# Kernel optimization log

Hardware: AMD Instinct MI355X
Metric: run time of the kernel (lower is better)

The kernel has to match this reference:

```python
import jax, jax.numpy as jnp
import numpy as np

N_NODES = 20000
N_EDGES = 160000
N_GRAPHS = 1000
IN_DIM = 11
HID = 128
EDGE_DIM = 3
N_LAYERS = 5
BN_EPS = 1e-5


def setup_inputs() -> dict:
    key = jax.random.key(0)
    ks = jax.random.split(key, 24)
    x = jax.random.normal(ks[0], (N_NODES, IN_DIM), dtype=jnp.float32)
    edge_index = jax.random.randint(ks[1], (2, N_EDGES), 0, N_NODES, dtype=jnp.int64)
    batch = jnp.sort(jax.random.randint(ks[2], (N_NODES,), 0, N_GRAPHS, dtype=jnp.int64))
    edge_attr = jax.random.uniform(ks[3], (N_EDGES, EDGE_DIM), dtype=jnp.float32)
    s_in = 1.0 / np.sqrt(IN_DIM)
    s_z = 1.0 / np.sqrt(2 * HID + EDGE_DIM)
    s_h = 1.0 / np.sqrt(HID)
    W_in = jax.random.uniform(ks[4], (IN_DIM, HID), minval=-s_in, maxval=s_in)
    b_in = jax.random.uniform(ks[5], (HID,), minval=-s_in, maxval=s_in)
    Wf = jax.random.uniform(ks[6], (N_LAYERS, 2 * HID + EDGE_DIM, HID), minval=-s_z, maxval=s_z)
    bf = jax.random.uniform(ks[7], (N_LAYERS, HID), minval=-s_z, maxval=s_z)
    Ws = jax.random.uniform(ks[8], (N_LAYERS, 2 * HID + EDGE_DIM, HID), minval=-s_z, maxval=s_z)
    bs = jax.random.uniform(ks[9], (N_LAYERS, HID), minval=-s_z, maxval=s_z)
    gamma = jnp.ones((N_LAYERS, HID), dtype=jnp.float32)
    beta = jnp.zeros((N_LAYERS, HID), dtype=jnp.float32)
    W1 = jax.random.uniform(ks[10], (HID, HID), minval=-s_h, maxval=s_h)
    b1 = jax.random.uniform(ks[11], (HID,), minval=-s_h, maxval=s_h)
    W2 = jax.random.uniform(ks[12], (HID, HID), minval=-s_h, maxval=s_h)
    b2 = jax.random.uniform(ks[13], (HID,), minval=-s_h, maxval=s_h)
    W3 = jax.random.uniform(ks[14], (HID, 1), minval=-s_h, maxval=s_h)
    b3 = jax.random.uniform(ks[15], (1,), minval=-s_h, maxval=s_h)
    return {"x": x, "edge_index": edge_index, "batch": batch, "edge_attr": edge_attr,
            "W_in": W_in, "b_in": b_in, "Wf": Wf, "bf": bf, "Ws": Ws, "bs": bs,
            "gamma": gamma, "beta": beta, "W1": W1, "b1": b1, "W2": W2, "b2": b2,
            "W3": W3, "b3": b3}


def reference(x, edge_index, batch, edge_attr, W_in, b_in, Wf, bf, Ws, bs,
              gamma, beta, W1, b1, W2, b2, W3, b3):
    src = edge_index[0]  # x_j (source / neighbor)
    dst = edge_index[1]  # x_i (target / aggregation index)
    # in-degree per node for mean aggregation (zero-degree -> divide by 1, yields 0)
    deg = jax.ops.segment_sum(jnp.ones((N_EDGES,), jnp.float32), dst, num_segments=N_NODES)
    deg = jnp.maximum(deg, 1.0)[:, None]

    h = x @ W_in + b_in  # [N, H]
    for l in range(N_LAYERS):
        # CGConv: z = [x_i, x_j, e]; msg = sigmoid(z Wf) * softplus(z Ws); residual + mean-aggr
        z = jnp.concatenate([h[dst], h[src], edge_attr], axis=-1)  # [E, 2H+D]
        msg = jax.nn.sigmoid(z @ Wf[l] + bf[l]) * jax.nn.softplus(z @ Ws[l] + bs[l])
        agg = jax.ops.segment_sum(msg, dst, num_segments=N_NODES) / deg
        h = h + agg
        # BatchNorm1d (training-mode batch stats, biased variance)
        mu = jnp.mean(h, axis=0)
        var = jnp.mean((h - mu) ** 2, axis=0)
        h = (h - mu) * jax.lax.rsqrt(var + BN_EPS) * gamma[l] + beta[l]
        h = jax.nn.relu(h)
        # dropout omitted (eval mode)

    # global mean pool over graphs
    cnt = jax.ops.segment_sum(jnp.ones((N_NODES,), jnp.float32), batch, num_segments=N_GRAPHS)
    g = jax.ops.segment_sum(h, batch, num_segments=N_GRAPHS) / jnp.maximum(cnt, 1.0)[:, None]

    g = jax.nn.relu(g @ W1 + b1)
    g = jax.nn.relu(g @ W2 + b2)
    return g @ W3 + b3  # [G, 1]
```

## Files before the change

### kernel.cpp

```cpp
#include <hip/hip_runtime.h>
#include <hip/hip_cooperative_groups.h>
#include <math.h>

namespace cg = cooperative_groups;

#define NN 20000
#define NE 160000
#define NG 1000
#define IND 11
#define H 128
#define ED 3
#define NL 5
#define ZDH (259*128)
#define BN_EPSF 1e-5f
#define EPW 32
#define QR 16
#define GP 4
#define MBLK 313
#define NWIN (NE / EPW)
#define MEGA_BLOCKS 1024

#define DEG_BLKS ((NE + 255) / 256)
#define WPREP_BLKS ((NL * 512 * H + 255) / 256)
#define GB_BLKS ((NN + 255) / 256)
#define HIN_BLKS 512
#define PREP_ITEMS (DEG_BLKS + WPREP_BLKS + GB_BLKS + HIN_BLKS)
#define RSV_ITEMS ((NN + 255) / 256)
#define SCAT_ITEMS ((NE + 255) / 256)
#define ZERO_INTS (NN + 1 + NE / 32)

typedef unsigned short ushort_t;
typedef unsigned int uint_t;
typedef __attribute__((ext_vector_type(8))) short bf8_t;
typedef __attribute__((ext_vector_type(4))) float f4_t;

__device__ inline ushort_t f2bf(float x) {
    unsigned int u = __float_as_uint(x);
    unsigned int r = (u + 0x7fffu + ((u >> 16) & 1u)) >> 16;
    return (ushort_t)r;
}
__device__ inline float bf2f(ushort_t b) {
    return __uint_as_float(((unsigned int)b) << 16);
}


__device__ __forceinline__ void prep_item(int b, int tid,
                                          const int* __restrict__ dst,
                                          int* __restrict__ degi,
                                          const float* __restrict__ Wf,
                                          const float* __restrict__ Ws,
                                          ushort_t* __restrict__ Wt,
                                          const float* __restrict__ x,
                                          const float* __restrict__ Win,
                                          const float* __restrict__ bin,
                                          float* __restrict__ h,
                                          const int* __restrict__ batch,
                                          int* __restrict__ gstart,
                                          float* lw ) {
    if (b < DEG_BLKS) {
        int e = b * 256 + tid;
        if (e < NE) atomicAdd(&degi[dst[e]], 1);
    } else if (b < DEG_BLKS + WPREP_BLKS) {
        int idx = (b - DEG_BLKS) * 256 + tid;
        if (idx < NL * 512 * H) {
            int k = idx & 127;
            int n = (idx >> 7) & 511;
            int l = idx >> 16;
            int t = n >> 7, j = n & 127;
            const float* W = (t == 0 || t == 2) ? Wf : Ws;
            int krow = (t < 2) ? k : (H + k);
            ushort_t val = f2bf(W[(size_t)l * ZDH + krow * H + j]);
            int nt = j >> 4, sub = j & 15;
            int ks = k >> 5, quad = (k >> 3) & 3, e2 = k & 7;
            int lane = quad * 16 + sub;
            Wt[(size_t)l * 65536 + (size_t)t * 16384 +
               (((nt * 4 + ks) * 64 + lane) * 8 + e2)] = val;
        }
    } else if (b < DEG_BLKS + WPREP_BLKS + GB_BLKS) {
        int n = (b - DEG_BLKS - WPREP_BLKS) * 256 + tid;
        if (n < NN) {
            int b0 = batch[n];
            int bn = (n + 1 < NN) ? batch[n + 1] : NG;
            if (n == 0)
                for (int t = 0; t <= b0; ++t) gstart[t] = 0;
            for (int t = b0 + 1; t <= bn; ++t) gstart[t] = n + 1;
        }
    } else {
        for (int i = tid; i < IND * H; i += 256) lw[i] = Win[i];
        __syncthreads();
        int j = tid & 127;
        float bj = bin[j];
        int rb = b - (DEG_BLKS + WPREP_BLKS + GB_BLKS);
        for (int n = rb * 2 + (tid >> 7); n < NN; n += HIN_BLKS * 2) {
            const float* xr = x + (size_t)n * IND;
            float acc = bj;
#pragma unroll
            for (int k = 0; k < IND; ++k) acc = fmaf(xr[k], lw[k * H + j], acc);
            h[(size_t)n * H + j] = acc;
        }
    }
}

__device__ __forceinline__ void reserve_item(int b, int tid,
                                             const int* __restrict__ degi,
                                             int* __restrict__ cursor,
                                             float* __restrict__ invdeg,
                                             int* __restrict__ counter,
                                             unsigned* __restrict__ endmask) {
    int n = b * 256 + tid;
    int lane = tid & 63;
    int v = (n < NN) ? degi[n] : 0;
    int x = v;
#pragma unroll
    for (int st = 1; st < 64; st <<= 1) {
        int y = __shfl_up(x, st, 64);
        if (lane >= st) x += y;
    }
    int total = __shfl(x, 63, 64);
    int base = 0;
    if (lane == 63) base = atomicAdd(counter, total);
    base = __shfl(base, 63, 64);
    if (n < NN) {
        int st0 = base + x - v;
        cursor[n] = st0;
        invdeg[n] = 1.0f / (float)(v < 1 ? 1 : v);
        if (v > 0) {
            int endp = st0 + v - 1;
            atomicOr(&endmask[endp >> 5], 1u << (endp & 31));
        }
    }
}

__device__ __forceinline__ void scatter_item(int b, int tid,
                                             const int* __restrict__ src,
                                             const int* __restrict__ dst,
                                             const float* __restrict__ ea,
                                             const float* __restrict__ invdeg,
                                             int* __restrict__ cursor,
                                             float4* __restrict__ csr_ea4,
                                             int* __restrict__ csr_dst,
                                             float* __restrict__ csr_inv) {
    int e = b * 256 + tid;
    if (e < NE) {
        int d = dst[e];
        int pos = atomicAdd(&cursor[d], 1);
        float4 r;
        r.x = ea[e * ED + 0];
        r.y = ea[e * ED + 1];
        r.z = ea[e * ED + 2];
        r.w = __int_as_float(src[e]);
        csr_ea4[pos] = r;
        csr_dst[pos] = d;
        csr_inv[pos] = invdeg[d];
    }
}

__device__ __forceinline__ void gemm_item(int mb, int pair,
                                          const float* __restrict__ hsrc,
                                          float* __restrict__ hbn,
                                          const ushort_t* __restrict__ Wt_l,
                                          const float* bnsc, const float* bnsh,
                                          int applyBN,
                                          uint_t* __restrict__ ppack,
                                          uint_t* __restrict__ qpack, int tid) {
    int wave = tid >> 6;
    int lane = tid & 63;
    int sub = lane & 15;
    int quad = lane >> 4;
    int m0 = mb * 64 + wave * 16;
    int writeH = applyBN && (pair == 0);

    const bf8_t* fragF = (const bf8_t*)(Wt_l + (size_t)(2 * pair) * 16384);
    const bf8_t* fragS = (const bf8_t*)(Wt_l + (size_t)(2 * pair + 1) * 16384);

    bf8_t aHi[4], aLo[4];
    int r = m0 + sub;
    int rc = r < NN ? r : NN - 1;
#pragma unroll
    for (int ks = 0; ks < 4; ++ks) {
        int kb = ks * 32 + quad * 8;
        const float* hp = hsrc + (size_t)rc * H + kb;
        float4 v0 = *(const float4*)hp;
        float4 v1 = *(const float4*)(hp + 4);
        float vv[8] = {v0.x, v0.y, v0.z, v0.w, v1.x, v1.y, v1.z, v1.w};
        if (applyBN) {
#pragma unroll
            for (int i = 0; i < 8; ++i) {
                float v = fmaf(vv[i], bnsc[kb + i], bnsh[kb + i]);
                vv[i] = v > 0.0f ? v : 0.0f;
            }
        }
        bf8_t hi8, lo8;
#pragma unroll
        for (int i = 0; i < 8; ++i) {
            ushort_t hi = f2bf(vv[i]);
            hi8[i] = (short)hi;
            lo8[i] = (short)f2bf(vv[i] - bf2f(hi));
        }
        aHi[ks] = hi8;
        aLo[ks] = lo8;
        if (writeH && r < NN) {
            float* op = hbn + (size_t)r * H + kb;
            *(float4*)op = make_float4(vv[0], vv[1], vv[2], vv[3]);
            *(float4*)(op + 4) = make_float4(vv[4], vv[5], vv[6], vv[7]);
        }
    }

    f4_t accF[8], accS[8];
#pragma unroll
    for (int b = 0; b < 8; ++b) { accF[b] = (f4_t){0.f, 0.f, 0.f, 0.f}; accS[b] = (f4_t){0.f, 0.f, 0.f, 0.f}; }

#pragma unroll
    for (int nt = 0; nt < 8; ++nt) {
#pragma unroll
        for (int ks = 0; ks < 4; ++ks) {
            bf8_t bF = fragF[(nt * 4 + ks) * 64 + lane];
            bf8_t bS = fragS[(nt * 4 + ks) * 64 + lane];
            accF[nt] = __builtin_amdgcn_mfma_f32_16x16x32_bf16(aHi[ks], bF, accF[nt], 0, 0, 0);
            accF[nt] = __builtin_amdgcn_mfma_f32_16x16x32_bf16(aLo[ks], bF, accF[nt], 0, 0, 0);
            accS[nt] = __builtin_amdgcn_mfma_f32_16x16x32_bf16(aHi[ks], bS, accS[nt], 0, 0, 0);
            accS[nt] = __builtin_amdgcn_mfma_f32_16x16x32_bf16(aLo[ks], bS, accS[nt], 0, 0, 0);
        }
    }

    uint_t* outp = pair ? qpack : ppack;
#pragma unroll
    for (int nt = 0; nt < 8; ++nt) {
        int col = nt * 16 + sub;
#pragma unroll
        for (int rr = 0; rr < 4; ++rr) {
            int row = m0 + quad * 4 + rr;
            if (row < NN) {
                uint_t lo = f2bf(accF[nt][rr]);
                uint_t hi = f2bf(accS[nt][rr]);
                outp[(size_t)row * H + col] = lo | (hi << 16);
            }
        }
    }
}

struct AggW { float2 wf0, wf1, wf2, ws0, ws1, ws2, bfv, bsv; };

__device__ __forceinline__ AggW load_aggw(const float* __restrict__ Wf_l,
                                          const float* __restrict__ bf_l,
                                          const float* __restrict__ Ws_l,
                                          const float* __restrict__ bs_l, int c0) {
    AggW a;
    a.wf0 = *(const float2*)&Wf_l[256 * H + c0];
    a.wf1 = *(const float2*)&Wf_l[257 * H + c0];
    a.wf2 = *(const float2*)&Wf_l[258 * H + c0];
    a.ws0 = *(const float2*)&Ws_l[256 * H + c0];
    a.ws1 = *(const float2*)&Ws_l[257 * H + c0];
    a.ws2 = *(const float2*)&Ws_l[258 * H + c0];
    a.bfv = *(const float2*)&bf_l[c0];
    a.bsv = *(const float2*)&bs_l[c0];
    return a;
}

__device__ __forceinline__ void agg_window(int base,
                                           const int4* __restrict__ csr_fe,
                                           const int* __restrict__ csr_dst,
                                           const float* __restrict__ csr_inv,
                                           const unsigned* __restrict__ endmask,
                                           const AggW& aw,
                                           const uint_t* __restrict__ ppack,
                                           const uint_t* __restrict__ qpack,
                                           float* __restrict__ h, int lane) {
    int c0 = 2 * lane;
    int4 fe = csr_fe[base + (lane & (EPW - 1))];
    int  dd = csr_dst[base + (lane & (EPW - 1))];
    int  ivr = __float_as_int(csr_inv[base + (lane & (EPW - 1))]);
    unsigned mask = __builtin_amdgcn_readfirstlane(endmask[base >> 5]);

    uint2 q[QR];
#pragma unroll
    for (int i = 0; i < QR; ++i) {
        int s = __builtin_amdgcn_readlane(fe.w, i);
        q[i] = *(const uint2*)&qpack[(size_t)s * H + c0];
    }

    int dcur = __builtin_amdgcn_readlane(dd, 0);
    uint2 ppc = *(const uint2*)&ppack[(size_t)dcur * H + c0];
    float pf0 = __uint_as_float(ppc.x << 16) + aw.bfv.x;
    float ps0 = __uint_as_float(ppc.x & 0xFFFF0000u) + aw.bsv.x;
    float pf1 = __uint_as_float(ppc.y << 16) + aw.bfv.y;
    float ps1 = __uint_as_float(ppc.y & 0xFFFF0000u) + aw.bsv.y;
    unsigned m = mask;
    int e0 = m ? __builtin_ctz(m) : EPW;
    int dnext = 0;
    uint2 ppN = ppc;
    if (e0 + 1 < EPW) {
        dnext = __builtin_amdgcn_readlane(dd, e0 + 1);
        ppN = *(const uint2*)&ppack[(size_t)dnext * H + c0];
    }

    float acc0 = 0.f, acc1 = 0.f;

#pragma unroll
    for (int tb = 0; tb < EPW; tb += 8) {
#pragma unroll
        for (int i = 0; i < 8; ++i) {
            int t = tb + i;
            float ex = __int_as_float(__builtin_amdgcn_readlane(fe.x, t));
            float ey = __int_as_float(__builtin_amdgcn_readlane(fe.y, t));
            float ez = __int_as_float(__builtin_amdgcn_readlane(fe.z, t));
            uint2 qq = q[t & (QR - 1)];
            if (t + QR < EPW) {
                int s2 = __builtin_amdgcn_readlane(fe.w, t + QR);
                q[t & (QR - 1)] = *(const uint2*)&qpack[(size_t)s2 * H + c0];
            }
            float qf0 = __uint_as_float(qq.x << 16);
            float qs0 = __uint_as_float(qq.x & 0xFFFF0000u);
            float qf1 = __uint_as_float(qq.y << 16);
            float qs1 = __uint_as_float(qq.y & 0xFFFF0000u);
            float f0 = fmaf(ex, aw.wf0.x, fmaf(ey, aw.wf1.x, fmaf(ez, aw.wf2.x, pf0 + qf0)));
            float v0 = fmaf(ex, aw.ws0.x, fmaf(ey, aw.ws1.x, fmaf(ez, aw.ws2.x, ps0 + qs0)));
            float f1 = fmaf(ex, aw.wf0.y, fmaf(ey, aw.wf1.y, fmaf(ez, aw.wf2.y, pf1 + qf1)));
            float v1 = fmaf(ex, aw.ws0.y, fmaf(ey, aw.ws1.y, fmaf(ez, aw.ws2.y, ps1 + qs1)));
            float sig0 = __builtin_amdgcn_rcpf(1.0f + __expf(-f0));
            float sp0  = fmaxf(v0, 0.0f) + __logf(1.0f + __expf(-fabsf(v0)));
            float sig1 = __builtin_amdgcn_rcpf(1.0f + __expf(-f1));
            float sp1  = fmaxf(v1, 0.0f) + __logf(1.0f + __expf(-fabsf(v1)));
            acc0 = fmaf(sig0, sp0, acc0);
            acc1 = fmaf(sig1, sp1, acc1);
            if (mask & (1u << t)) {
                float inv = __int_as_float(__builtin_amdgcn_readlane(ivr, t));
                atomicAdd(&h[(size_t)dcur * H + c0], acc0 * inv);
                atomicAdd(&h[(size_t)dcur * H + c0 + 1], acc1 * inv);
                acc0 = 0.f; acc1 = 0.f;
                dcur = dnext;
                pf0 = __uint_as_float(ppN.x << 16) + aw.bfv.x;
                ps0 = __uint_as_float(ppN.x & 0xFFFF0000u) + aw.bsv.x;
                pf1 = __uint_as_float(ppN.y << 16) + aw.bfv.y;
                ps1 = __uint_as_float(ppN.y & 0xFFFF0000u) + aw.bsv.y;
                m &= m - 1;
                int e1 = m ? __builtin_ctz(m) : EPW;
                if (e1 + 1 < EPW) {
                    dnext = __builtin_amdgcn_readlane(dd, e1 + 1);
                    ppN = *(const uint2*)&ppack[(size_t)dnext * H + c0];
                }
            }
        }
    }
    if (!(mask & (1u << (EPW - 1)))) {
        float inv = __int_as_float(__builtin_amdgcn_readlane(ivr, EPW - 1));
        atomicAdd(&h[(size_t)dcur * H + c0], acc0 * inv);
        atomicAdd(&h[(size_t)dcur * H + c0 + 1], acc1 * inv);
    }
}

__device__ __forceinline__ void stats_part(const float* __restrict__ h,
                                           float* __restrict__ sum,
                                           float* __restrict__ sumsq,
                                           int j, int part, int nparts) {
    float s = 0.0f, ss = 0.0f;
    for (int n = part * 8; n + 7 < NN; n += nparts * 8) {
        float v[8];
#pragma unroll
        for (int i = 0; i < 8; ++i) v[i] = h[(size_t)(n + i) * H + j];
#pragma unroll
        for (int i = 0; i < 8; ++i) { s += v[i]; ss = fmaf(v[i], v[i], ss); }
    }
    atomicAdd(&sum[j], s);
    atomicAdd(&sumsq[j], ss);
}

__global__ __launch_bounds__(256, 4) void mega_kernel(
        const int* __restrict__ src, const int* __restrict__ dst,
        const float* __restrict__ ea, const float* __restrict__ x,
        const float* __restrict__ Win, const float* __restrict__ bin,
        const int* __restrict__ batch,
        int* __restrict__ degi, int* __restrict__ counter,
        unsigned* __restrict__ endmask, int* __restrict__ cursor,
        float* __restrict__ invdeg, float4* __restrict__ csr_ea4,
        int* __restrict__ csr_dst, float* __restrict__ csr_inv,
        int* __restrict__ gstart,
        const float* __restrict__ Wf, const float* __restrict__ bf,
        const float* __restrict__ Ws, const float* __restrict__ bs,
        ushort_t* __restrict__ Wt,
        float* __restrict__ hA, float* __restrict__ hB,
        uint_t* __restrict__ ppack, uint_t* __restrict__ qpack,
        float* __restrict__ sum, float* __restrict__ sumsq,
        const float* __restrict__ gamma, const float* __restrict__ beta,
        const float* __restrict__ W1, const float* __restrict__ b1,
        const float* __restrict__ W2, const float* __restrict__ b2,
        const float* __restrict__ W3, const float* __restrict__ b3,
        float* __restrict__ out) {
    cg::grid_group grid = cg::this_grid();
    __shared__ float bnsc[H];
    __shared__ float bnsh[H];
    __shared__ float lw[IND * H];
    __shared__ float s1[GP][H];
    __shared__ float s2[GP][H];
    __shared__ float wred[2][GP];
    int tid = threadIdx.x;
    int lane = tid & 63;
    int wv = tid >> 6;

    for (int i = blockIdx.x * 256 + tid; i < ZERO_INTS; i += gridDim.x * 256)
        degi[i] = 0;
    grid.sync();

    for (int item = blockIdx.x; item < PREP_ITEMS; item += gridDim.x) {
        prep_item(item, tid, dst, degi, Wf, Ws, Wt, x, Win, bin, hA, batch,
                  gstart, lw);
        __syncthreads();
    }
    grid.sync();

    for (int item = blockIdx.x; item < RSV_ITEMS; item += gridDim.x)
        reserve_item(item, tid, degi, cursor, invdeg, counter, endmask);
    grid.sync();

    for (int item = blockIdx.x; item < SCAT_ITEMS; item += gridDim.x)
        scatter_item(item, tid, src, dst, ea, invdeg, cursor,
                     csr_ea4, csr_dst, csr_inv);
    grid.sync();

    const int4* csr_fe = (const int4*)csr_ea4;

    for (int l = 0; l < NL; ++l) {
        const float* hsrc = (l == 0) ? hA : ((l & 1) ? hA : hB);
        float* hTgt = (l == 0) ? hA : ((l & 1) ? hB : hA);
        const ushort_t* Wt_l = Wt + (size_t)l * 512 * H;
        int applyBN = (l > 0);

        if (applyBN) {
            if (tid < H) {
                float mu  = sum[tid] * (1.0f / NN);
                float var = sumsq[tid] * (1.0f / NN) - mu * mu;
                float sc  = gamma[(size_t)(l - 1) * H + tid] * rsqrtf(var + BN_EPSF);
                bnsc[tid] = sc;
                bnsh[tid] = beta[(size_t)(l - 1) * H + tid] - mu * sc;
            }
            __syncthreads();
        }
        for (int item = blockIdx.x; item < 2 * MBLK; item += gridDim.x) {
            int pair = item >= MBLK;
            gemm_item(pair ? item - MBLK : item, pair, hsrc, hTgt, Wt_l,
                      bnsc, bnsh, applyBN, ppack, qpack, tid);
        }
        grid.sync();

        if (blockIdx.x == 0 && tid < H) { sum[tid] = 0.0f; sumsq[tid] = 0.0f; }
        {
            AggW aw = load_aggw(Wf + (size_t)l * ZDH, bf + (size_t)l * H,
                                Ws + (size_t)l * ZDH, bs + (size_t)l * H, 2 * lane);
            for (int w = blockIdx.x * 4 + wv; w < NWIN; w += gridDim.x * 4)
                agg_window(w * EPW, csr_fe, csr_dst, csr_inv, endmask, aw,
                           ppack, qpack, hTgt, lane);
        }
        grid.sync();

        if (blockIdx.x < 256)
            stats_part(hTgt, sum, sumsq, tid & 127, blockIdx.x * 2 + (tid >> 7), 512);
        grid.sync();
    }

    if (blockIdx.x < NG / GP) {
        const float* h = hA;
        const float* gam = gamma + (size_t)(NL - 1) * H;
        const float* bet = beta + (size_t)(NL - 1) * H;
        int j = tid;
        if (j < H) {
            float mu  = sum[j] * (1.0f / NN);
            float var = sumsq[j] * (1.0f / NN) - mu * mu;
            float sc  = gam[j] * rsqrtf(var + BN_EPSF);
            float sh  = bet[j] - mu * sc;
#pragma unroll
            for (int gi = 0; gi < GP; ++gi) {
                int g0 = blockIdx.x * GP + gi;
                int a = gstart[g0], e = gstart[g0 + 1];
                float p0 = 0.f, p1 = 0.f, p2 = 0.f, p3 = 0.f;
                int n = a;
                for (; n + 3 < e; n += 4) {
                    float v0 = fmaf(h[(size_t)(n + 0) * H + j], sc, sh);
                    float v1 = fmaf(h[(size_t)(n + 1) * H + j], sc, sh);
                    float v2 = fmaf(h[(size_t)(n + 2) * H + j], sc, sh);
                    float v3 = fmaf(h[(size_t)(n + 3) * H + j], sc, sh);
                    p0 += fmaxf(v0, 0.f); p1 += fmaxf(v1, 0.f);
                    p2 += fmaxf(v2, 0.f); p3 += fmaxf(v3, 0.f);
                }
                for (; n < e; ++n) {
                    float v = fmaf(h[(size_t)n * H + j], sc, sh);
                    p0 += fmaxf(v, 0.f);
                }
                float cf = (float)(e - a);
                if (cf < 1.f) cf = 1.f;
                s1[gi][j] = ((p0 + p1) + (p2 + p3)) / cf;
            }
        }
        __syncthreads();

        float a1[GP];
        if (j < H) {
#pragma unroll
            for (int gi = 0; gi < GP; ++gi) a1[gi] = b1[j];
            for (int k = 0; k < H; ++k) {
                float w = W1[k * H + j];
#pragma unroll
                for (int gi = 0; gi < GP; ++gi) a1[gi] = fmaf(s1[gi][k], w, a1[gi]);
            }
#pragma unroll
            for (int gi = 0; gi < GP; ++gi) s2[gi][j] = fmaxf(a1[gi], 0.f);
        }
        __syncthreads();

        if (j < H) {
#pragma unroll
            for (int gi = 0; gi < GP; ++gi) a1[gi] = b2[j];
            for (int k = 0; k < H; ++k) {
                float w = W2[k * H + j];
#pragma unroll
                for (int gi = 0; gi < GP; ++gi) a1[gi] = fmaf(s2[gi][k], w, a1[gi]);
            }
            float w3 = W3[j];
#pragma unroll
            for (int gi = 0; gi < GP; ++gi) {
                float p = fmaxf(a1[gi], 0.f) * w3;
                for (int off2 = 32; off2 > 0; off2 >>= 1) p += __shfl_down(p, off2, 64);
                if ((j & 63) == 0) wred[j >> 6][gi] = p;
            }
        }
        __syncthreads();
        if (tid < GP) out[blockIdx.x * GP + tid] = wred[0][tid] + wred[1][tid] + b3[0];
    }
}

__global__ __launch_bounds__(256) void prep_fused(const int* __restrict__ dst,
                                                  int* __restrict__ degi,
                                                  const float* __restrict__ Wf,
                                                  const float* __restrict__ Ws,
                                                  ushort_t* __restrict__ Wt,
                                                  const float* __restrict__ x,
                                                  const float* __restrict__ Win,
                                                  const float* __restrict__ bin,
                                                  float* __restrict__ h,
                                                  const int* __restrict__ batch,
                                                  int* __restrict__ gstart) {
    __shared__ float lw[IND * H];
    prep_item(blockIdx.x, threadIdx.x, dst, degi, Wf, Ws, Wt, x, Win, bin, h,
              batch, gstart, lw);
}

__global__ __launch_bounds__(256) void reserve_kernel(const int* __restrict__ degi,
                                                      int* __restrict__ cursor,
                                                      float* __restrict__ invdeg,
                                                      int* __restrict__ counter,
                                                      unsigned* __restrict__ endmask) {
    reserve_item(blockIdx.x, threadIdx.x, degi, cursor, invdeg, counter, endmask);
}

__global__ void scatter_kernel(const int* __restrict__ src, const int* __restrict__ dst,
                               const float* __restrict__ ea,
                               const float* __restrict__ invdeg,
                               int* __restrict__ cursor, float4* __restrict__ csr_ea4,
                               int* __restrict__ csr_dst, float* __restrict__ csr_inv) {
    scatter_item(blockIdx.x, threadIdx.x, src, dst, ea, invdeg, cursor,
                 csr_ea4, csr_dst, csr_inv);
}

__global__ __launch_bounds__(256, 4) void node_gemm_mfma(const float* __restrict__ hsrc,
                                                         float* __restrict__ hbn,
                                                         const ushort_t* __restrict__ Wt_l,
                                                         const float* __restrict__ sum,
                                                         const float* __restrict__ sumsq,
                                                         const float* __restrict__ gamma_l,
                                                         const float* __restrict__ beta_l,
                                                         int applyBN,
                                                         uint_t* __restrict__ ppack,
                                                         uint_t* __restrict__ qpack) {
    __shared__ float bnsc[H];
    __shared__ float bnsh[H];
    int tid = threadIdx.x;
    if (applyBN) {
        if (tid < H) {
            float mu  = sum[tid] * (1.0f / NN);
            float var = sumsq[tid] * (1.0f / NN) - mu * mu;
            float sc  = gamma_l[tid] * rsqrtf(var + BN_EPSF);
            bnsc[tid] = sc;
            bnsh[tid] = beta_l[tid] - mu * sc;
        }
        __syncthreads();
    }
    gemm_item(blockIdx.x, blockIdx.y, hsrc, hbn, Wt_l, bnsc, bnsh,
              applyBN, ppack, qpack, tid);
}

__global__ __launch_bounds__(256) void agg_edge_kernel(const int4* __restrict__ csr_fe,
                                                       const int* __restrict__ csr_dst,
                                                       const float* __restrict__ csr_inv,
                                                       const unsigned* __restrict__ endmask,
                                                       const float* __restrict__ Wf_l,
                                                       const float* __restrict__ bf_l,
                                                       const float* __restrict__ Ws_l,
                                                       const float* __restrict__ bs_l,
                                                       const uint_t* __restrict__ ppack,
                                                       const uint_t* __restrict__ qpack,
                                                       float* __restrict__ h,
                                                       float* __restrict__ sum,
                                                       float* __restrict__ sumsq) {
    int tid = threadIdx.x;
    if (blockIdx.x == 0 && tid < H) { sum[tid] = 0.0f; sumsq[tid] = 0.0f; }
    int lane = tid & 63;
    int wv = tid >> 6;
    AggW aw = load_aggw(Wf_l, bf_l, Ws_l, bs_l, 2 * lane);
    agg_window((blockIdx.x * 4 + wv) * EPW, csr_fe, csr_dst, csr_inv, endmask, aw,
               ppack, qpack, h, lane);
}

__global__ __launch_bounds__(H) void stats_kernel(const float* __restrict__ h,
                                                  float* __restrict__ sum,
                                                  float* __restrict__ sumsq) {
    stats_part(h, sum, sumsq, threadIdx.x, blockIdx.x, gridDim.x);
}

__global__ __launch_bounds__(H) void pool_mlp_kernel(const float* __restrict__ h,
                                                     const int* __restrict__ gstart,
                                                     const float* __restrict__ sum,
                                                     const float* __restrict__ sumsq,
                                                     const float* __restrict__ gamma,
                                                     const float* __restrict__ beta,
                                                     const float* __restrict__ W1,
                                                     const float* __restrict__ b1,
                                                     const float* __restrict__ W2,
                                                     const float* __restrict__ b2,
                                                     const float* __restrict__ W3,
                                                     const float* __restrict__ b3,
                                                     float* __restrict__ out) {
    int j = threadIdx.x;
    float mu  = sum[j] * (1.0f / NN);
    float var = sumsq[j] * (1.0f / NN) - mu * mu;
    float sc  = gamma[j] * rsqrtf(var + BN_EPSF);
    float sh  = beta[j] - mu * sc;

    __shared__ float s1[GP][H];
    __shared__ float s2[GP][H];

#pragma unroll
    for (int gi = 0; gi < GP; ++gi) {
        int g0 = blockIdx.x * GP + gi;
        int a = gstart[g0], e = gstart[g0 + 1];
        float p0 = 0.f, p1 = 0.f, p2 = 0.f, p3 = 0.f;
        int n = a;
        for (; n + 3 < e; n += 4) {
            float v0 = fmaf(h[(size_t)(n + 0) * H + j], sc, sh);
            float v1 = fmaf(h[(size_t)(n + 1) * H + j], sc, sh);
            float v2 = fmaf(h[(size_t)(n + 2) * H + j], sc, sh);
            float v3 = fmaf(h[(size_t)(n + 3) * H + j], sc, sh);
            p0 += fmaxf(v0, 0.f); p1 += fmaxf(v1, 0.f);
            p2 += fmaxf(v2, 0.f); p3 += fmaxf(v3, 0.f);
        }
        for (; n < e; ++n) {
            float v = fmaf(h[(size_t)n * H + j], sc, sh);
            p0 += fmaxf(v, 0.f);
        }
        float cf = (float)(e - a);
        if (cf < 1.f) cf = 1.f;
        s1[gi][j] = ((p0 + p1) + (p2 + p3)) / cf;
    }
    __syncthreads();

    float a1[GP];
#pragma unroll
    for (int gi = 0; gi < GP; ++gi) a1[gi] = b1[j];
    for (int k = 0; k < H; ++k) {
        float w = W1[k * H + j];
#pragma unroll
        for (int gi = 0; gi < GP; ++gi) a1[gi] = fmaf(s1[gi][k], w, a1[gi]);
    }
#pragma unroll
    for (int gi = 0; gi < GP; ++gi) s2[gi][j] = fmaxf(a1[gi], 0.f);
    __syncthreads();

#pragma unroll
    for (int gi = 0; gi < GP; ++gi) a1[gi] = b2[j];
    for (int k = 0; k < H; ++k) {
        float w = W2[k * H + j];
#pragma unroll
        for (int gi = 0; gi < GP; ++gi) a1[gi] = fmaf(s2[gi][k], w, a1[gi]);
    }

    float w3 = W3[j];
    __shared__ float wred[2][GP];
#pragma unroll
    for (int gi = 0; gi < GP; ++gi) {
        float p = fmaxf(a1[gi], 0.f) * w3;
        for (int off2 = 32; off2 > 0; off2 >>= 1) p += __shfl_down(p, off2, 64);
        if ((j & 63) == 0) wred[j >> 6][gi] = p;
    }
    __syncthreads();
    if (j < GP) out[blockIdx.x * GP + j] = wred[0][j] + wred[1][j] + b3[0];
}

extern "C" void kernel_launch(void* const* d_in, const int* in_sizes, int n_in,
                              void* d_out, int out_size, void* d_ws, size_t ws_size,
                              hipStream_t stream) {
    const float* x     = (const float*)d_in[0];
    const int*   ei    = (const int*)d_in[1];
    const int*   srcp  = ei;
    const int*   dstp  = ei + NE;
    const int*   batch = (const int*)d_in[2];
    const float* ea    = (const float*)d_in[3];
    const float* Win   = (const float*)d_in[4];
    const float* bin   = (const float*)d_in[5];
    const float* Wf    = (const float*)d_in[6];
    const float* bf    = (const float*)d_in[7];
    const float* Ws    = (const float*)d_in[8];
    const float* bs    = (const float*)d_in[9];
    const float* gamma = (const float*)d_in[10];
    const float* beta  = (const float*)d_in[11];
    const float* W1    = (const float*)d_in[12];
    const float* b1    = (const float*)d_in[13];
    const float* W2    = (const float*)d_in[14];
    const float* b2    = (const float*)d_in[15];
    const float* W3    = (const float*)d_in[16];
    const float* b3    = (const float*)d_in[17];
    float* out = (float*)d_out;

    const size_t NH = (size_t)NN * H;
    float* wsp = (float*)d_ws;
    size_t off = 0;
    float* hA     = wsp + off; off += NH;
    float* hB     = wsp + off; off += NH;
    uint_t* ppack = (uint_t*)(wsp + off); off += NH;
    uint_t* qpack = (uint_t*)(wsp + off); off += NH;
    float* invdeg = wsp + off; off += NN;
    float* sum    = wsp + off; off += H;
    float* sumsq  = wsp + off; off += H;
    int* gstart   = (int*)(wsp + off); off += NG + 1;
    off = (off + 3) & ~(size_t)3;
    float4* csr_ea4 = (float4*)(wsp + off); off += (size_t)NE * 4;
    float* csr_inv = wsp + off; off += NE;
    int* degi      = (int*)(wsp + off); off += NN;
    int* counter   = (int*)(wsp + off); off += 1;
    unsigned* endmask = (unsigned*)(wsp + off); off += NE / 32;
    int* cursor    = (int*)(wsp + off); off += NN;
    int* csr_dst   = (int*)(wsp + off); off += NE;
    off = (off + 3) & ~(size_t)3;
    ushort_t* Wt = (ushort_t*)(wsp + off); off += (size_t)NL * 512 * H / 2;

    static int megaOK = -1;
    if (megaOK < 0) {
        int nb = 0;
        hipError_t oe = hipOccupancyMaxActiveBlocksPerMultiprocessor(&nb, mega_kernel, 256, 0);
        megaOK = (oe == hipSuccess && nb >= 4) ? 1 : 0;
    }
    bool megaDone = false;
    if (megaOK) {
        const int* src_p = srcp; const int* dst_p = dstp;
        const float* ea_p = ea; const float* x_p = x;
        const float* Win_p = Win; const float* bin_p = bin;
        const int* batch_p = batch;
        int* degi_p = degi; int* counter_p = counter;
        unsigned* endmask_p = endmask; int* cursor_p = cursor;
        float* invdeg_p = invdeg; float4* csr_ea4_p = csr_ea4;
        int* csr_dst_p = csr_dst; float* csr_inv_p = csr_inv;
        int* gstart_p = gstart;
        const float* Wf_p = Wf; const float* bf_p = bf;
        const float* Ws_p = Ws; const float* bs_p = bs;
        ushort_t* Wt_p = Wt;
        float* hA_p = hA; float* hB_p = hB;
        uint_t* pp_p = ppack; uint_t* qp_p = qpack;
        float* sum_p = sum; float* sumsq_p = sumsq;
        const float* gamma_p = gamma; const float* beta_p = beta;
        const float* W1_p = W1; const float* b1_p = b1;
        const float* W2_p = W2; const float* b2_p = b2;
        const float* W3_p = W3; const float* b3_p = b3;
        float* out_p = out;
        void* margs[] = {&src_p, &dst_p, &ea_p, &x_p, &Win_p, &bin_p, &batch_p,
                         &degi_p, &counter_p, &endmask_p, &cursor_p,
                         &invdeg_p, &csr_ea4_p, &csr_dst_p, &csr_inv_p, &gstart_p,
                         &Wf_p, &bf_p, &Ws_p, &bs_p, &Wt_p,
                         &hA_p, &hB_p, &pp_p, &qp_p, &sum_p, &sumsq_p,
                         &gamma_p, &beta_p,
                         &W1_p, &b1_p, &W2_p, &b2_p, &W3_p, &b3_p, &out_p};
        hipError_t merr = hipLaunchCooperativeKernel(mega_kernel, dim3(MEGA_BLOCKS),
                                                     dim3(256), margs, 0, stream);
        if (merr == hipSuccess) megaDone = true;
        else (void)hipGetLastError();
    }

    if (!megaDone) {
        hipMemsetAsync(degi, 0, ZERO_INTS * sizeof(int), stream);
        prep_fused<<<PREP_ITEMS, 256, 0, stream>>>(dstp, degi, Wf, Ws, Wt,
                                                   x, Win, bin, hA, batch, gstart);
        reserve_kernel<<<RSV_ITEMS, 256, 0, stream>>>(degi, cursor, invdeg, counter,
                                                      endmask);
        scatter_kernel<<<SCAT_ITEMS, 256, 0, stream>>>(srcp, dstp, ea, invdeg, cursor,
                                                       csr_ea4, csr_dst, csr_inv);
        float* hRead = hA;
        for (int l = 0; l < NL; ++l) {
            float* hTgt = (l == 0) ? hA : ((l & 1) ? hB : hA);
            node_gemm_mfma<<<dim3(MBLK, 2), 256, 0, stream>>>(
                hRead, hTgt, Wt + (size_t)l * 512 * H, sum, sumsq,
                gamma + (size_t)(l ? l - 1 : 0) * H,
                beta  + (size_t)(l ? l - 1 : 0) * H,
                l > 0, ppack, qpack);
            agg_edge_kernel<<<NWIN / 4, 256, 0, stream>>>((const int4*)csr_ea4, csr_dst,
                                                          csr_inv, endmask,
                                                          Wf + (size_t)l * ZDH, bf + (size_t)l * H,
                                                          Ws + (size_t)l * ZDH, bs + (size_t)l * H,
                                                          ppack, qpack, hTgt, sum, sumsq);
            stats_kernel<<<512, H, 0, stream>>>(hTgt, sum, sumsq);
            hRead = hTgt;
        }
        pool_mlp_kernel<<<NG / GP, H, 0, stream>>>(hRead, gstart, sum, sumsq,
                                                   gamma + (size_t)(NL - 1) * H,
                                                   beta + (size_t)(NL - 1) * H,
                                                   W1, b1, W2, b2, W3, b3, out);
    }
}
```

Measured before the change: 457.0 us.

## Replace cooperative grid syncs with custom atomic barrier and merge zeroing with prep

Swaps most cg grid.sync calls for a hand-written global barrier, an atomic counter with s_sleep polling. The counter is zeroed in the same pass as degi and stays monotonic within a launch. The non-degree prep work (weight conversion, graph starts, input projection) moves into the zeroing phase, so one grid-wide barrier fewer is needed before the degree count. This aims to cut barrier overhead across about 19 grid syncs. In exchange it relies on hand-written memory fences, and the barrier may be less robust than the library implementation.

Result: no change. 454.9 us (-0.5%).

```diff
diff --git a/kernel.cpp b/kernel.cpp
--- a/kernel.cpp
+++ b/kernel.cpp
@@ -27,7 +27,9 @@
 #define PREP_ITEMS (DEG_BLKS + WPREP_BLKS + GB_BLKS + HIN_BLKS)
 #define RSV_ITEMS ((NN + 255) / 256)
 #define SCAT_ITEMS ((NE + 255) / 256)
-#define ZERO_INTS (NN + 1 + NE / 32)
+#define ZERO_INTS (NN + 1 + NE / 32 + 16)
+#define ZERO_ITEMS ((ZERO_INTS + 255) / 256)
+#define P0_ITEMS (ZERO_ITEMS + WPREP_BLKS + GB_BLKS + HIN_BLKS)
 
 typedef unsigned short ushort_t;
 typedef unsigned int uint_t;
@@ -41,6 +43,21 @@
 }
 __device__ inline float bf2f(ushort_t b) {
     return __uint_as_float(((unsigned int)b) << 16);
+}
+
+__device__ __forceinline__ void gbar_sync(unsigned* bar, unsigned nb, int tid) {
+    __syncthreads();
+    if (tid == 0) {
+        __threadfence();
+        unsigned old = __hip_atomic_fetch_add(bar, 1u, __ATOMIC_ACQ_REL,
+                                              __HIP_MEMORY_SCOPE_AGENT);
+        unsigned target = (old / nb + 1u) * nb;
+        while (__hip_atomic_load(bar, __ATOMIC_ACQUIRE,
+                                 __HIP_MEMORY_SCOPE_AGENT) < target)
+            __builtin_amdgcn_s_sleep(8);
+        __threadfence();
+    }
+    __syncthreads();
 }
 
 
@@ -371,7 +388,8 @@
         const float* __restrict__ Win, const float* __restrict__ bin,
         const int* __restrict__ batch,
         int* __restrict__ degi, int* __restrict__ counter,
-        unsigned* __restrict__ endmask, int* __restrict__ cursor,
+        unsigned* __restrict__ endmask, unsigned* __restrict__ gbar,
+        int* __restrict__ cursor,
         float* __restrict__ invdeg, float4* __restrict__ csr_ea4,
         int* __restrict__ csr_dst, float* __restrict__ csr_inv,
         int* __restrict__ gstart,
@@ -396,26 +414,33 @@
     int tid = threadIdx.x;
     int lane = tid & 63;
     int wv = tid >> 6;
-
-    for (int i = blockIdx.x * 256 + tid; i < ZERO_INTS; i += gridDim.x * 256)
-        degi[i] = 0;
+    unsigned nb = gridDim.x;
+
+    for (int item = blockIdx.x; item < P0_ITEMS; item += gridDim.x) {
+        if (item < ZERO_ITEMS) {
+            int i0 = item * 256 + tid;
+            if (i0 < ZERO_INTS) degi[i0] = 0;
+        } else {
+            prep_item(DEG_BLKS + (item - ZERO_ITEMS), tid, dst, degi, Wf, Ws,
+                      Wt, x, Win, bin, hA, batch, gstart, lw);
+        }
+        __syncthreads();
+    }
     grid.sync();
 
-    for (int item = blockIdx.x; item < PREP_ITEMS; item += gridDim.x) {
+    for (int item = blockIdx.x; item < DEG_BLKS; item += gridDim.x)
         prep_item(item, tid, dst, degi, Wf, Ws, Wt, x, Win, bin, hA, batch,
                   gstart, lw);
-        __syncthreads();
-    }
-    grid.sync();
+    gbar_sync(gbar, nb, tid);
 
     for (int item = blockIdx.x; item < RSV_ITEMS; item += gridDim.x)
         reserve_item(item, tid, degi, cursor, invdeg, counter, endmask);
-    grid.sync();
+    gbar_sync(gbar, nb, tid);
 
     for (int item = blockIdx.x; item < SCAT_ITEMS; item += gridDim.x)
         scatter_item(item, tid, src, dst, ea, invdeg, cursor,
                      csr_ea4, csr_dst, csr_inv);
-    grid.sync();
+    gbar_sync(gbar, nb, tid);
 
     const int4* csr_fe = (const int4*)csr_ea4;
 
@@ -440,7 +465,7 @@
             gemm_item(pair ? item - MBLK : item, pair, hsrc, hTgt, Wt_l,
                       bnsc, bnsh, applyBN, ppack, qpack, tid);
         }
-        grid.sync();
+        gbar_sync(gbar, nb, tid);
 
         if (blockIdx.x == 0 && tid < H) { sum[tid] = 0.0f; sumsq[tid] = 0.0f; }
         {
@@ -450,11 +475,11 @@
                 agg_window(w * EPW, csr_fe, csr_dst, csr_inv, endmask, aw,
                            ppack, qpack, hTgt, lane);
         }
-        grid.sync();
+        gbar_sync(gbar, nb, tid);
 
         if (blockIdx.x < 256)
             stats_part(hTgt, sum, sumsq, tid & 127, blockIdx.x * 2 + (tid >> 7), 512);
-        grid.sync();
+        gbar_sync(gbar, nb, tid);
     }
 
     if (blockIdx.x < NG / GP) {
@@ -735,6 +760,7 @@
     int* degi      = (int*)(wsp + off); off += NN;
     int* counter   = (int*)(wsp + off); off += 1;
     unsigned* endmask = (unsigned*)(wsp + off); off += NE / 32;
+    unsigned* gbar = (unsigned*)(wsp + off); off += 16;
     int* cursor    = (int*)(wsp + off); off += NN;
     int* csr_dst   = (int*)(wsp + off); off += NE;
     off = (off + 3) & ~(size_t)3;
@@ -753,7 +779,8 @@
         const float* Win_p = Win; const float* bin_p = bin;
         const int* batch_p = batch;
         int* degi_p = degi; int* counter_p = counter;
-        unsigned* endmask_p = endmask; int* cursor_p = cursor;
+        unsigned* endmask_p = endmask; unsigned* gbar_p = gbar;
+        int* cursor_p = cursor;
         float* invdeg_p = invdeg; float4* csr_ea4_p = csr_ea4;
         int* csr_dst_p = csr_dst; float* csr_inv_p = csr_inv;
         int* gstart_p = gstart;
@@ -769,7 +796,7 @@
         const float* W3_p = W3; const float* b3_p = b3;
         float* out_p = out;
         void* margs[] = {&src_p, &dst_p, &ea_p, &x_p, &Win_p, &bin_p, &batch_p,
-                         &degi_p, &counter_p, &endmask_p, &cursor_p,
+                         &degi_p, &counter_p, &endmask_p, &gbar_p, &cursor_p,
                          &invdeg_p, &csr_ea4_p, &csr_dst_p, &csr_inv_p, &gstart_p,
                          &Wf_p, &bf_p, &Ws_p, &bs_p, &Wt_p,
                          &hA_p, &hB_p, &pp_p, &qp_p, &sum_p, &sumsq_p,
```
